# Kernel optimization log

Hardware: AMD Instinct MI355X
Metric: run time of the kernel (lower is better)

Reference implementation:

```python
import jax, jax.numpy as jnp
import numpy as np

N, G, NPG, K = 65536, 64, 1024, 32
NB, BD, IN_CH, GNN_DIM, L = 64, 4, 256, 256, 2
NBP = (BD - 1) * BD // 2 * NB  # 384
E = 524288


def setup_inputs():
    key = jax.random.key(0)
    ks = jax.random.split(key, 10)
    s = 0.05
    return {
        "x": jax.random.normal(ks[0], (N, IN_CH), jnp.float32),
        "eigvec": jax.random.normal(ks[1], (N, K), jnp.float32) / np.float32(np.sqrt(NPG)),
        "eigval": jax.random.uniform(ks[2], (G, K), jnp.float32, 0.0, 2.0),
        "taus": jnp.ones((NB,), jnp.float32),
        "enc_w": jax.random.normal(ks[3], (IN_CH, GNN_DIM), jnp.float32) * s,
        "enc_b": jnp.zeros((GNN_DIM,), jnp.float32),
        "self_w": jax.random.normal(ks[4], (L, GNN_DIM, GNN_DIM), jnp.float32) * s,
        "self_b": jnp.zeros((L, GNN_DIM), jnp.float32),
        "nb_w": jax.random.normal(ks[5], (L, GNN_DIM, GNN_DIM), jnp.float32) * s,
        "nb_b": jnp.zeros((L, GNN_DIM), jnp.float32),
        "dec_w": jax.random.normal(ks[6], (GNN_DIM, NBP), jnp.float32) * s,
        "dec_b": jnp.zeros((NBP,), jnp.float32),
        "lin_w": jax.random.normal(ks[7], (IN_CH, IN_CH), jnp.float32) * s,
        "lin_b": jnp.zeros((IN_CH,), jnp.float32),
        "edge_index": jax.random.randint(ks[8], (2, E), 0, N, jnp.int32),
    }


def _householder(p):
    # p: [M, BD*(BD-1)//2] -> Q: [M, BD, BD], product of BD-1 Householder reflectors
    M = p.shape[0]
    Q = jnp.broadcast_to(jnp.eye(BD, dtype=p.dtype), (M, BD, BD))
    idx = 0
    for j in range(BD - 1):  # small fixed loop over bundle_dim-1 reflectors
        n = BD - 1 - j
        v = jnp.zeros((M, BD), p.dtype).at[:, j].set(1.0)
        v = v.at[:, j + 1:].set(p[:, idx:idx + n])
        idx += n
        nrm = jnp.sum(v * v, axis=1)[:, None, None]
        Qv = jnp.einsum('mij,mj->mi', Q, v)
        Q = Q - 2.0 * Qv[:, :, None] * v[:, None, :] / nrm
    return Q


def reference(x, eigvec, eigval, taus, enc_w, enc_b, self_w, self_b,
              nb_w, nb_b, dec_w, dec_b, lin_w, lin_b, edge_index):
    gelu = lambda t: jax.nn.gelu(t, approximate=False)
    src, dst = edge_index[0], edge_index[1]
    vf = x.reshape(N, NB, BD, -1)                      # [N, NB, BD, 1]
    # SumGNN structural encoder: h = gelu(enc(x)); residual GNN layers; dec
    h = gelu(x @ enc_w + enc_b)
    for k in range(L):
        agg = jax.ops.segment_sum(h[src], dst, num_segments=N)  # sum aggregation
        hk = (h @ self_w[k] + self_b[k]) + (agg @ nb_w[k] + nb_b[k])
        h = gelu(hk) + h
    node_rep = h @ dec_w + dec_b                       # [N, NBP]
    Q = _householder(node_rep.reshape(N * NB, NBP // NB)).reshape(N, NB, BD, BD)
    vf = jnp.einsum('abcd,abde->abce', Q, vf)          # bundle transform
    h = vf.reshape(G, NPG, IN_CH)                      # to_dense_batch (equal-size graphs)
    ev = eigvec.reshape(G, NPG, K)
    hs = jnp.einsum('gnv,gnd->gvd', ev, h)             # project onto eigenbasis
    fact = jnp.exp(-eigval[:, :, None] * taus[None, None, :])   # [G, K, NB]
    hs = (hs.reshape(G, K, NB, BD, -1) * fact[..., None, None]).reshape(G, K, IN_CH)
    h = jnp.einsum('gnv,gvd->gnd', ev, hs).reshape(N, IN_CH)     # reproject
    h = h @ lin_w + lin_b
    vf = jnp.einsum('abdc,abde->abce', Q, h.reshape(N, NB, BD, -1))  # Q^T
    return vf.reshape(N, IN_CH)
```

## Files before the change

### kernel.cpp

```cpp
#include <hip/hip_runtime.h>
#include <math.h>

#define NN      65536
#define GG      64
#define NPG     1024
#define KEIG    32
#define NBUN    64
#define BDIM    4
#define CH      256
#define NBP     384
#define NEDGE   524288

using f16x8 = __attribute__((ext_vector_type(8))) _Float16;
using f16x4 = __attribute__((ext_vector_type(4))) _Float16;
using f32x4 = __attribute__((ext_vector_type(4))) float;

__device__ __forceinline__ float gelu_f(float x) {
    return 0.5f * x * (1.0f + erff(x * 0.70710678118654752440f));
}

template<int NOUT, int KTOT, bool DUAL, bool ACT, bool RESA, bool WF, bool W16>
__global__ __launch_bounds__(NOUT, 3) void mgemm_k(
    const _Float16* __restrict__ A1, const _Float16* __restrict__ A2,
    const _Float16* __restrict__ Bp, const float* __restrict__ bias,
    float* __restrict__ Cf, _Float16* __restrict__ C16)
{
    constexpr int NT   = KTOT / 32;
    constexpr int HALVES = KTOT / 256;
    constexpr int ROWB = 512;
    constexpr int CPR  = 32;
    constexpr int TOTC = 64 * CPR;
    constexpr int NSTG = TOTC / NOUT;
    constexpr int CTS  = NOUT + 8;
    constexpr int AH   = 64 * 256;
    constexpr int CTH  = 64 * CTS;
    constexpr int LDSH = (W16 && CTH > AH) ? CTH : AH;
    __shared__ _Float16 Alds[LDSH];

    const int tid  = threadIdx.x;
    const int lane = tid & 63;
    const int wave = tid >> 6;
    const int m0   = blockIdx.x * 64;

    const int r16 = lane & 15;
    const int kc  = lane >> 4;

    const _Float16* bpp = Bp + ((size_t)wave * NT * 2048) + lane * 8;

    f16x8 pa0, pa1, pa2, pa3, pb0, pb1, pb2, pb3;
    f16x8 pc0, pc1, pc2, pc3, pd0, pd1, pd2, pd3;

#define LDB(P0, P1, P2, P3, T)                                                 \
    {                                                                          \
        const _Float16* bq_ = bpp + (size_t)(T) * 2048;                        \
        P0 = *(const f16x8*)(bq_);                                             \
        P1 = *(const f16x8*)(bq_ + 512);                                       \
        P2 = *(const f16x8*)(bq_ + 1024);                                      \
        P3 = *(const f16x8*)(bq_ + 1536);                                      \
    }

    auto stage = [&](const _Float16* __restrict__ BASE) {
#pragma unroll
        for (int j0 = 0; j0 < NSTG; j0 += 4) {
            f16x8 s0, s1, s2, s3;
            const int nv = (NSTG - j0 >= 4) ? 4 : (NSTG - j0);
            int i0 = tid + (j0 + 0) * NOUT;
            int i1 = tid + (j0 + 1) * NOUT;
            int i2 = tid + (j0 + 2) * NOUT;
            int i3 = tid + (j0 + 3) * NOUT;
            if (nv > 0) s0 = *(const f16x8*)(BASE + (size_t)(m0 + (i0 >> 5)) * 256 + (i0 & 31) * 8);
            if (nv > 1) s1 = *(const f16x8*)(BASE + (size_t)(m0 + (i1 >> 5)) * 256 + (i1 & 31) * 8);
            if (nv > 2) s2 = *(const f16x8*)(BASE + (size_t)(m0 + (i2 >> 5)) * 256 + (i2 & 31) * 8);
            if (nv > 3) s3 = *(const f16x8*)(BASE + (size_t)(m0 + (i3 >> 5)) * 256 + (i3 & 31) * 8);
            if (nv > 0) *(f16x8*)((char*)Alds + ((((i0 >> 5) * ROWB + (i0 & 31) * 16)) ^ (((i0 >> 5) & 7) << 4))) = s0;
            if (nv > 1) *(f16x8*)((char*)Alds + ((((i1 >> 5) * ROWB + (i1 & 31) * 16)) ^ (((i1 >> 5) & 7) << 4))) = s1;
            if (nv > 2) *(f16x8*)((char*)Alds + ((((i2 >> 5) * ROWB + (i2 & 31) * 16)) ^ (((i2 >> 5) & 7) << 4))) = s2;
            if (nv > 3) *(f16x8*)((char*)Alds + ((((i3 >> 5) * ROWB + (i3 & 31) * 16)) ^ (((i3 >> 5) & 7) << 4))) = s3;
        }
        if (TOTC % NOUT) {
            const int idx = tid + NSTG * NOUT;
            if (idx < TOTC) {
                const int r = idx >> 5, c = idx & 31;
                f16x8 v = *(const f16x8*)(BASE + (size_t)(m0 + r) * 256 + c * 8);
                *(f16x8*)((char*)Alds + ((r * ROWB + c * 16) ^ ((r & 7) << 4))) = v;
            }
        }
    };

    LDB(pa0, pa1, pa2, pa3, 0)
    LDB(pb0, pb1, pb2, pb3, 1)
    LDB(pc0, pc1, pc2, pc3, 2)
    LDB(pd0, pd1, pd2, pd3, 3)

    stage(A1);
    __syncthreads();

    f32x4 acc[4][4];
#pragma unroll
    for (int i = 0; i < 4; i++)
#pragma unroll
        for (int j = 0; j < 4; j++) acc[i][j] = 0.f;

#define MSTEP(OFF, P0, P1, P2, P3)                                             \
    {                                                                          \
        const char* ap_ = (const char*)Alds + (OFF);                           \
        f16x8 a0_ = *(const f16x8*)(ap_);                                      \
        f16x8 a1_ = *(const f16x8*)(ap_ + 16 * ROWB);                          \
        f16x8 a2_ = *(const f16x8*)(ap_ + 32 * ROWB);                          \
        f16x8 a3_ = *(const f16x8*)(ap_ + 48 * ROWB);                          \
        acc[0][0] = __builtin_amdgcn_mfma_f32_16x16x32_f16(a0_, P0, acc[0][0], 0, 0, 0); \
        acc[0][1] = __builtin_amdgcn_mfma_f32_16x16x32_f16(a0_, P1, acc[0][1], 0, 0, 0); \
        acc[0][2] = __builtin_amdgcn_mfma_f32_16x16x32_f16(a0_, P2, acc[0][2], 0, 0, 0); \
        acc[0][3] = __builtin_amdgcn_mfma_f32_16x16x32_f16(a0_, P3, acc[0][3], 0, 0, 0); \
        acc[1][0] = __builtin_amdgcn_mfma_f32_16x16x32_f16(a1_, P0, acc[1][0], 0, 0, 0); \
        acc[1][1] = __builtin_amdgcn_mfma_f32_16x16x32_f16(a1_, P1, acc[1][1], 0, 0, 0); \
        acc[1][2] = __builtin_amdgcn_mfma_f32_16x16x32_f16(a1_, P2, acc[1][2], 0, 0, 0); \
        acc[1][3] = __builtin_amdgcn_mfma_f32_16x16x32_f16(a1_, P3, acc[1][3], 0, 0, 0); \
        acc[2][0] = __builtin_amdgcn_mfma_f32_16x16x32_f16(a2_, P0, acc[2][0], 0, 0, 0); \
        acc[2][1] = __builtin_amdgcn_mfma_f32_16x16x32_f16(a2_, P1, acc[2][1], 0, 0, 0); \
        acc[2][2] = __builtin_amdgcn_mfma_f32_16x16x32_f16(a2_, P2, acc[2][2], 0, 0, 0); \
        acc[2][3] = __builtin_amdgcn_mfma_f32_16x16x32_f16(a2_, P3, acc[2][3], 0, 0, 0); \
        acc[3][0] = __builtin_amdgcn_mfma_f32_16x16x32_f16(a3_, P0, acc[3][0], 0, 0, 0); \
        acc[3][1] = __builtin_amdgcn_mfma_f32_16x16x32_f16(a3_, P1, acc[3][1], 0, 0, 0); \
        acc[3][2] = __builtin_amdgcn_mfma_f32_16x16x32_f16(a3_, P2, acc[3][2], 0, 0, 0); \
        acc[3][3] = __builtin_amdgcn_mfma_f32_16x16x32_f16(a3_, P3, acc[3][3], 0, 0, 0); \
    }

    const int swz = (r16 & 7) << 4;
#pragma unroll
    for (int h = 0; h < HALVES; ++h) {
        if (h > 0) {
            __syncthreads();
            stage(A2);
            __syncthreads();
        }
        int au = r16 * ROWB + kc * 16;
#pragma unroll
        for (int tt = 0; tt < 8; tt += 4) {
            const int t = h * 8 + tt;
            MSTEP((au      ) ^ swz, pa0, pa1, pa2, pa3)
            if (t + 4 < NT) LDB(pa0, pa1, pa2, pa3, t + 4)
            MSTEP((au +  64) ^ swz, pb0, pb1, pb2, pb3)
            if (t + 5 < NT) LDB(pb0, pb1, pb2, pb3, t + 5)
            MSTEP((au + 128) ^ swz, pc0, pc1, pc2, pc3)
            if (t + 6 < NT) LDB(pc0, pc1, pc2, pc3, t + 6)
            MSTEP((au + 192) ^ swz, pd0, pd1, pd2, pd3)
            if (t + 7 < NT) LDB(pd0, pd1, pd2, pd3, t + 7)
            au += 256;
        }
    }
#undef LDB
#undef MSTEP

    const int rbase = (lane >> 4) * 4;
    const int ncol  = lane & 15;
    if constexpr (W16) {
        __syncthreads();
        constexpr int CPRN = NOUT / 8;
        constexpr int CPT  = 64 * CPRN / NOUT;
        f16x8 res[CPT];
        if constexpr (RESA) {
#pragma unroll
            for (int k2 = 0; k2 < CPT; k2++) {
                const int c = tid + k2 * NOUT;
                const int row = c / CPRN, col = c - row * CPRN;
                res[k2] = *(const f16x8*)(A1 + (size_t)(m0 + row) * 256 + col * 8);
            }
        }
#pragma unroll
        for (int nt = 0; nt < 4; nt++) {
            const int n = wave * 64 + nt * 16 + ncol;
            const float bs = bias[n];
#pragma unroll
            for (int mt = 0; mt < 4; mt++) {
#pragma unroll
                for (int i = 0; i < 4; i++) {
                    const int mr = mt * 16 + rbase + i;
                    float v = acc[mt][nt][i] + bs;
                    if (ACT) v = gelu_f(v);
                    Alds[mr * CTS + n] = (_Float16)v;
                }
            }
        }
        __syncthreads();
#pragma unroll
        for (int k2 = 0; k2 < CPT; k2++) {
            const int c = tid + k2 * NOUT;
            const int row = c / CPRN, col = c - row * CPRN;
            f16x8 v = *(const f16x8*)&Alds[row * CTS + col * 8];
            if constexpr (RESA) v = v + res[k2];
            *(f16x8*)(C16 + (size_t)(m0 + row) * NOUT + col * 8) = v;
        }
    } else {
#pragma unroll
        for (int nt = 0; nt < 4; nt++) {
            const int n = wave * 64 + nt * 16 + ncol;
            const float bs = bias[n];
#pragma unroll
            for (int mt = 0; mt < 4; mt++) {
#pragma unroll
                for (int i = 0; i < 4; i++) {
                    const int m = m0 + mt * 16 + rbase + i;
                    float v = acc[mt][nt][i] + bs;
                    if (ACT) v = gelu_f(v);
                    if (RESA) v += (float)A1[(size_t)m * 256 + n];
                    if (WF) Cf[(size_t)m * NOUT + n] = v;
                }
            }
        }
    }
}

template<int NOUT, int KTOT, bool DUAL>
__global__ __launch_bounds__(256) void pack_k(
    const float* __restrict__ W1, const float* __restrict__ W2,
    _Float16* __restrict__ Bp)
{
    constexpr int NT = KTOT / 32;
    const int cid = blockIdx.x * 256 + threadIdx.x;
    if (cid >= NOUT * KTOT / 8) return;
    const int l  = cid & 63;
    const int q  = (cid >> 6) & 3;
    const int c2 = cid >> 8;
    const int t  = c2 & (NT - 1);
    const int wn = c2 / NT;
    const int n  = wn * 64 + q * 16 + (l & 15);
    const int k0 = t * 32 + (l >> 4) * 8;
    f16x8 v;
#pragma unroll
    for (int j = 0; j < 8; j++) {
        const int k = k0 + j;
        float w = (DUAL && k >= 256) ? W2[(size_t)(k - 256) * NOUT + n]
                                     : W1[(size_t)k * NOUT + n];
        v[j] = (_Float16)w;
    }
    *(f16x8*)(Bp + (size_t)cid * 8) = v;
}

__global__ void zero_k(float* __restrict__ p, size_t n)
{
    size_t i = (size_t)blockIdx.x * blockDim.x + threadIdx.x;
    float4* p4 = (float4*)p;
    size_t n4 = n >> 2;
    for (size_t j = i; j < n4; j += (size_t)gridDim.x * blockDim.x)
        p4[j] = make_float4(0.f, 0.f, 0.f, 0.f);
}

__global__ __launch_bounds__(256) void cvt16_k(
    const float* __restrict__ in, _Float16* __restrict__ out)
{
    size_t i = (size_t)blockIdx.x * 256 + threadIdx.x;
    float4 v = ((const float4*)in)[i];
    f16x4 o = { (_Float16)v.x, (_Float16)v.y, (_Float16)v.z, (_Float16)v.w };
    ((f16x4*)out)[i] = o;
}

__global__ void bcomb_k(const float* __restrict__ a, const float* __restrict__ b,
                        float* __restrict__ o)
{
    int i = blockIdx.x * 256 + threadIdx.x;
    if (i < 512) o[i] = a[i] + b[i];
}

__global__ __launch_bounds__(256) void hist_k(const int* __restrict__ ei, int* __restrict__ deg)
{
    int e = blockIdx.x * 256 + threadIdx.x;
    if (e < NEDGE) atomicAdd(&deg[ei[NEDGE + e]], 1);
}

__global__ __launch_bounds__(1024) void scan_k(
    const int* __restrict__ deg, int* __restrict__ off, int* __restrict__ cursor)
{
    __shared__ int sh[1024];
    const int tid = threadIdx.x;
    const int base = tid * 64;
    int s = 0;
#pragma unroll 8
    for (int i = 0; i < 64; i++) s += deg[base + i];
    const int mysum = s;
    sh[tid] = s;
    __syncthreads();
    for (int ofs = 1; ofs < 1024; ofs <<= 1) {
        int v = (tid >= ofs) ? sh[tid - ofs] : 0;
        __syncthreads();
        sh[tid] += v;
        __syncthreads();
    }
    int running = sh[tid] - mysum;
    for (int i = 0; i < 64; i++) {
        off[base + i] = running;
        cursor[base + i] = running;
        running += deg[base + i];
    }
    if (tid == 1023) off[NN] = running;
}

__global__ __launch_bounds__(256) void fill_k(
    const int* __restrict__ ei, int* __restrict__ cursor, int* __restrict__ csr)
{
    int e = blockIdx.x * 256 + threadIdx.x;
    if (e < NEDGE) {
        int d = ei[NEDGE + e];
        int pos = atomicAdd(&cursor[d], 1);
        csr[pos] = ei[e];
    }
}

__global__ __launch_bounds__(256) void gather16_k(
    const _Float16* __restrict__ h, const int* __restrict__ off,
    const int* __restrict__ csr, _Float16* __restrict__ agg)
{
    const int lane = threadIdx.x & 63;
    const int n = blockIdx.x * 4 + (threadIdx.x >> 6);
    const int s0 = off[n], s1 = off[n + 1];
    float a0 = 0.f, a1 = 0.f, a2 = 0.f, a3 = 0.f;
    int j = s0;
    for (; j + 3 < s1; j += 4) {
        const int i0 = csr[j], i1 = csr[j + 1], i2 = csr[j + 2], i3 = csr[j + 3];
        f16x4 v0 = ((const f16x4*)(h + (size_t)i0 * CH))[lane];
        f16x4 v1 = ((const f16x4*)(h + (size_t)i1 * CH))[lane];
        f16x4 v2 = ((const f16x4*)(h + (size_t)i2 * CH))[lane];
        f16x4 v3 = ((const f16x4*)(h + (size_t)i3 * CH))[lane];
        a0 += (float)v0[0] + (float)v1[0] + (float)v2[0] + (float)v3[0];
        a1 += (float)v0[1] + (float)v1[1] + (float)v2[1] + (float)v3[1];
        a2 += (float)v0[2] + (float)v1[2] + (float)v2[2] + (float)v3[2];
        a3 += (float)v0[3] + (float)v1[3] + (float)v2[3] + (float)v3[3];
    }
    for (; j < s1; j++) {
        f16x4 va = ((const f16x4*)(h + (size_t)csr[j] * CH))[lane];
        a0 += (float)va[0]; a1 += (float)va[1]; a2 += (float)va[2]; a3 += (float)va[3];
    }
    f16x4 o = { (_Float16)a0, (_Float16)a1, (_Float16)a2, (_Float16)a3 };
    ((f16x4*)(agg + (size_t)n * CH))[lane] = o;
}

__device__ __forceinline__ void make_Q(const _Float16* __restrict__ p, float Q[4][4])
{
#pragma unroll
    for (int i = 0; i < 4; i++)
#pragma unroll
        for (int j = 0; j < 4; j++) Q[i][j] = (i == j) ? 1.f : 0.f;
    int idx = 0;
#pragma unroll
    for (int j = 0; j < 3; j++) {
        float v[4] = {0.f, 0.f, 0.f, 0.f};
        v[j] = 1.f;
#pragma unroll
        for (int t = 0; t < 4; t++)
            if (t > j) v[t] = (float)p[idx + t - (j + 1)];
        idx += 3 - j;
        float nrm = v[0]*v[0] + v[1]*v[1] + v[2]*v[2] + v[3]*v[3];
        float s = 2.f / nrm;
#pragma unroll
        for (int i = 0; i < 4; i++) {
            float qv = Q[i][0]*v[0] + Q[i][1]*v[1] + Q[i][2]*v[2] + Q[i][3]*v[3];
            float t0 = s * qv;
#pragma unroll
            for (int c = 0; c < 4; c++) Q[i][c] -= t0 * v[c];
        }
    }
}

template<bool TRANS>
__global__ __launch_bounds__(256) void bundle_k(
    const float* __restrict__ vin, const _Float16* __restrict__ nr,
    float* __restrict__ out)
{
    __shared__ _Float16 pb[4 * NBP];
    const int n0 = blockIdx.x * 4;
    for (int i = threadIdx.x; i < 4 * NBP; i += 256)
        pb[i] = nr[(size_t)n0 * NBP + i];
    __syncthreads();
    const int ln = threadIdx.x >> 6;
    const int b  = threadIdx.x & 63;
    const int n  = n0 + ln;
    float Q[4][4];
    make_Q(&pb[ln * NBP + b * 6], Q);
    float4 xv = ((const float4*)(vin + (size_t)n * CH))[b];
    float in0 = xv.x, in1 = xv.y, in2 = xv.z, in3 = xv.w;
    float4 o;
    if constexpr (!TRANS) {
        o.x = Q[0][0]*in0 + Q[0][1]*in1 + Q[0][2]*in2 + Q[0][3]*in3;
        o.y = Q[1][0]*in0 + Q[1][1]*in1 + Q[1][2]*in2 + Q[1][3]*in3;
        o.z = Q[2][0]*in0 + Q[2][1]*in1 + Q[2][2]*in2 + Q[2][3]*in3;
        o.w = Q[3][0]*in0 + Q[3][1]*in1 + Q[3][2]*in2 + Q[3][3]*in3;
    } else {
        o.x = Q[0][0]*in0 + Q[1][0]*in1 + Q[2][0]*in2 + Q[3][0]*in3;
        o.y = Q[0][1]*in0 + Q[1][1]*in1 + Q[2][1]*in2 + Q[3][1]*in3;
        o.z = Q[0][2]*in0 + Q[1][2]*in1 + Q[2][2]*in2 + Q[3][2]*in3;
        o.w = Q[0][3]*in0 + Q[1][3]*in1 + Q[2][3]*in2 + Q[3][3]*in3;
    }
    ((float4*)(out + (size_t)n * CH))[b] = o;
}

__global__ __launch_bounds__(256) void spec_proj_k(
    const float* __restrict__ v, const float* __restrict__ eigvec, float* __restrict__ hs)
{
    const int g = blockIdx.x;
    const int nbase = g * NPG + blockIdx.y * 128;
    __shared__ float evs[16][32];
    float acc[32];
#pragma unroll
    for (int k = 0; k < 32; k++) acc[k] = 0.f;
    for (int nt = 0; nt < 128; nt += 16) {
        __syncthreads();
        for (int i = threadIdx.x; i < 512; i += 256) {
            int nn = i >> 5, kk = i & 31;
            evs[nn][kk] = eigvec[(size_t)(nbase + nt + nn) * KEIG + kk];
        }
        __syncthreads();
#pragma unroll 4
        for (int nn = 0; nn < 16; nn++) {
            float hv = v[(size_t)(nbase + nt + nn) * CH + threadIdx.x];
#pragma unroll
            for (int k = 0; k < 32; k++) acc[k] += evs[nn][k] * hv;
        }
    }
    float* o = hs + (size_t)g * KEIG * CH + threadIdx.x;
#pragma unroll
    for (int k = 0; k < 32; k++) atomicAdd(o + k * CH, acc[k]);
}

__global__ __launch_bounds__(256) void spec_reproj16_k(
    const float* __restrict__ eigvec, const float* __restrict__ hs,
    const float* __restrict__ eigval, const float* __restrict__ taus,
    _Float16* __restrict__ out16)
{
    const int g = blockIdx.x >> 4;
    const int nbase = g * NPG + (blockIdx.x & 15) * 64;
    const float tau = taus[threadIdx.x >> 2];
    float hsr[32];
    const float* hg = hs + (size_t)g * KEIG * CH + threadIdx.x;
#pragma unroll
    for (int k = 0; k < 32; k++)
        hsr[k] = hg[k * CH] * expf(-eigval[g * KEIG + k] * tau);
    __shared__ float evs[64][32];
    for (int i = threadIdx.x; i < 2048; i += 256) {
        int nn = i >> 5, kk = i & 31;
        evs[nn][kk] = eigvec[(size_t)(nbase + nn) * KEIG + kk];
    }
    __syncthreads();
    for (int nn = 0; nn < 64; nn++) {
        float a = 0.f;
#pragma unroll
        for (int k = 0; k < 32; k++) a += evs[nn][k] * hsr[k];
        out16[(size_t)(nbase + nn) * CH + threadIdx.x] = (_Float16)a;
    }
}

extern "C" void kernel_launch(void* const* d_in, const int* in_sizes, int n_in,
                              void* d_out, int out_size, void* d_ws, size_t ws_size,
                              hipStream_t stream)
{
    const float* x      = (const float*)d_in[0];
    const float* eigvec = (const float*)d_in[1];
    const float* eigval = (const float*)d_in[2];
    const float* taus   = (const float*)d_in[3];
    const float* enc_w  = (const float*)d_in[4];
    const float* enc_b  = (const float*)d_in[5];
    const float* self_w = (const float*)d_in[6];
    const float* self_b = (const float*)d_in[7];
    const float* nb_w   = (const float*)d_in[8];
    const float* nb_b   = (const float*)d_in[9];
    const float* dec_w  = (const float*)d_in[10];
    const float* dec_b  = (const float*)d_in[11];
    const float* lin_w  = (const float*)d_in[12];
    const float* lin_b  = (const float*)d_in[13];
    const int*   ei     = (const int*)d_in[14];
    (void)in_sizes; (void)n_in; (void)out_size; (void)ws_size;

    float* ws = (float*)d_ws;
    _Float16* x16 = (_Float16*)(ws);
    _Float16* h0  = (_Float16*)(ws + 8388608);
    _Float16* h1  = (_Float16*)(ws + 16777216);
    _Float16* agg = (_Float16*)(ws + 25165824);
    int* ibase  = (int*)(ws + 33554432);
    int* deg    = ibase;
    int* off    = ibase + 65536;
    int* cursor = ibase + 131073;
    int* csr    = ibase + 196609;
    _Float16* nr16 = (_Float16*)(ws + 25165824);
    float* wb = ws + 37748752;
    _Float16* enc16 = (_Float16*)(wb);
    _Float16* l1w   = (_Float16*)(wb + 32768);
    _Float16* l2w   = (_Float16*)(wb + 98304);
    _Float16* dec16 = (_Float16*)(wb + 163840);
    _Float16* lin16 = (_Float16*)(wb + 212992);
    float* lbias = wb + 245760;
    _Float16* h2 = (_Float16*)(ws + 37995024);
    float* vf1 = ws;
    float* hs  = ws + 16777216;
    float* h3  = vf1;

    dim3 blk(256);

    cvt16_k<<<16384, blk, 0, stream>>>(x, x16);
    pack_k<256, 256, false><<<32, blk, 0, stream>>>(enc_w, nullptr, enc16);
    pack_k<256, 512, true ><<<64, blk, 0, stream>>>(self_w,         nb_w,         l1w);
    pack_k<256, 512, true ><<<64, blk, 0, stream>>>(self_w + 65536, nb_w + 65536, l2w);
    pack_k<384, 256, false><<<48, blk, 0, stream>>>(dec_w, nullptr, dec16);
    pack_k<256, 256, false><<<32, blk, 0, stream>>>(lin_w, nullptr, lin16);
    bcomb_k<<<2, blk, 0, stream>>>(self_b, nb_b, lbias);
    zero_k<<<64, blk, 0, stream>>>((float*)deg, (size_t)NN);
    hist_k<<<NEDGE / 256, blk, 0, stream>>>(ei, deg);
    scan_k<<<1, 1024, 0, stream>>>(deg, off, cursor);
    fill_k<<<NEDGE / 256, blk, 0, stream>>>(ei, cursor, csr);

    mgemm_k<256, 256, false, true, false, false, true><<<dim3(1024), blk, 0, stream>>>(
        x16, nullptr, enc16, enc_b, nullptr, h0);

    gather16_k<<<NN / 4, blk, 0, stream>>>(h0, off, csr, agg);
    mgemm_k<256, 512, true, true, true, false, true><<<dim3(1024), blk, 0, stream>>>(
        h0, agg, l1w, lbias, nullptr, h1);

    gather16_k<<<NN / 4, blk, 0, stream>>>(h1, off, csr, agg);
    mgemm_k<256, 512, true, true, true, false, true><<<dim3(1024), blk, 0, stream>>>(
        h1, agg, l2w, lbias + 256, nullptr, h0);

    mgemm_k<384, 256, false, false, false, false, true><<<dim3(1024), dim3(384), 0, stream>>>(
        h0, nullptr, dec16, dec_b, nullptr, nr16);

    bundle_k<false><<<NN / 4, blk, 0, stream>>>(x, nr16, vf1);

    zero_k<<<512, blk, 0, stream>>>(hs, (size_t)GG * KEIG * CH);
    spec_proj_k<<<dim3(GG, 8), blk, 0, stream>>>(vf1, eigvec, hs);
    spec_reproj16_k<<<GG * 16, blk, 0, stream>>>(eigvec, hs, eigval, taus, h2);

    mgemm_k<256, 256, false, false, false, true, false><<<dim3(1024), blk, 0, stream>>>(
        h2, nullptr, lin16, lin_b, h3, nullptr);

    bundle_k<true><<<NN / 4, blk, 0, stream>>>(h3, nr16, (float*)d_out);
}
```

Measured before the change: 688.5 us.

## Fuse fp32→fp16 conversion and bundle transforms into GEMM kernels

Removes the standalone x-to-fp16 conversion by loading fp32 A directly in the encoder GEMM. It fuses the forward bundle transform into the decoder GEMM epilogue, building Q from the tile still in LDS and writing vf as fp16. It also fuses the Q^T bundle transform into the final linear GEMM epilogue, staging fp32 results in LDS. This cuts several full-size global round trips and kernel launches. In exchange, the epilogues get heavier, LDS use grows, and the spectral projection now reads fp16 vf, which lowers precision.

Result: faster. 637.5 us (-7.4%).

```diff
diff --git a/kernel.cpp b/kernel.cpp
--- a/kernel.cpp
+++ b/kernel.cpp
@@ -19,11 +19,40 @@
     return 0.5f * x * (1.0f + erff(x * 0.70710678118654752440f));
 }
 
-template<int NOUT, int KTOT, bool DUAL, bool ACT, bool RESA, bool WF, bool W16>
+__device__ __forceinline__ void make_Q(const _Float16* __restrict__ p, float Q[4][4])
+{
+#pragma unroll
+    for (int i = 0; i < 4; i++)
+#pragma unroll
+        for (int j = 0; j < 4; j++) Q[i][j] = (i == j) ? 1.f : 0.f;
+    int idx = 0;
+#pragma unroll
+    for (int j = 0; j < 3; j++) {
+        float v[4] = {0.f, 0.f, 0.f, 0.f};
+        v[j] = 1.f;
+#pragma unroll
+        for (int t = 0; t < 4; t++)
+            if (t > j) v[t] = (float)p[idx + t - (j + 1)];
+        idx += 3 - j;
+        float nrm = v[0]*v[0] + v[1]*v[1] + v[2]*v[2] + v[3]*v[3];
+        float s = 2.f / nrm;
+#pragma unroll
+        for (int i = 0; i < 4; i++) {
+            float qv = Q[i][0]*v[0] + Q[i][1]*v[1] + Q[i][2]*v[2] + Q[i][3]*v[3];
+            float t0 = s * qv;
+#pragma unroll
+            for (int c = 0; c < 4; c++) Q[i][c] -= t0 * v[c];
+        }
+    }
+}
+
+template<int NOUT, int KTOT, bool DUAL, bool ACT, bool RESA, bool W16, bool A32, int BUN>
 __global__ __launch_bounds__(NOUT, 3) void mgemm_k(
     const _Float16* __restrict__ A1, const _Float16* __restrict__ A2,
-    const _Float16* __restrict__ Bp, const float* __restrict__ bias,
-    float* __restrict__ Cf, _Float16* __restrict__ C16)
+    const float* __restrict__ A1f, const _Float16* __restrict__ Bp,
+    const float* __restrict__ bias, _Float16* __restrict__ C16,
+    const float* __restrict__ xin, _Float16* __restrict__ vf16,
+    const _Float16* __restrict__ nrq, float* __restrict__ outf)
 {
     constexpr int NT   = KTOT / 32;
     constexpr int HALVES = KTOT / 256;
@@ -33,8 +62,10 @@
     constexpr int NSTG = TOTC / NOUT;
     constexpr int CTS  = NOUT + 8;
     constexpr int AH   = 64 * 256;
-    constexpr int CTH  = 64 * CTS;
-    constexpr int LDSH = (W16 && CTH > AH) ? CTH : AH;
+    constexpr int W16H = W16 ? 64 * CTS : 0;
+    constexpr int B2H  = (BUN == 2) ? 64 * CTS * 2 : 0;
+    constexpr int LDSH = (AH > W16H) ? ((AH > B2H) ? AH : B2H)
+                                     : ((W16H > B2H) ? W16H : B2H);
     __shared__ _Float16 Alds[LDSH];
 
     const int tid  = threadIdx.x;
@@ -59,7 +90,20 @@
         P3 = *(const f16x8*)(bq_ + 1536);                                      \
     }
 
-    auto stage = [&](const _Float16* __restrict__ BASE) {
+    auto ldA = [&](const _Float16* B16, const float* B32, int idx) -> f16x8 {
+        const size_t off = (size_t)(m0 + (idx >> 5)) * 256 + (idx & 31) * 8;
+        if constexpr (A32) {
+            float4 lo = *(const float4*)(B32 + off);
+            float4 hi = *(const float4*)(B32 + off + 4);
+            f16x8 r = { (_Float16)lo.x, (_Float16)lo.y, (_Float16)lo.z, (_Float16)lo.w,
+                        (_Float16)hi.x, (_Float16)hi.y, (_Float16)hi.z, (_Float16)hi.w };
+            return r;
+        } else {
+            return *(const f16x8*)(B16 + off);
+        }
+    };
+
+    auto stage = [&](const _Float16* B16, const float* B32) {
 #pragma unroll
         for (int j0 = 0; j0 < NSTG; j0 += 4) {
             f16x8 s0, s1, s2, s3;
@@ -68,10 +112,10 @@
             int i1 = tid + (j0 + 1) * NOUT;
             int i2 = tid + (j0 + 2) * NOUT;
             int i3 = tid + (j0 + 3) * NOUT;
-            if (nv > 0) s0 = *(const f16x8*)(BASE + (size_t)(m0 + (i0 >> 5)) * 256 + (i0 & 31) * 8);
-            if (nv > 1) s1 = *(const f16x8*)(BASE + (size_t)(m0 + (i1 >> 5)) * 256 + (i1 & 31) * 8);
-            if (nv > 2) s2 = *(const f16x8*)(BASE + (size_t)(m0 + (i2 >> 5)) * 256 + (i2 & 31) * 8);
-            if (nv > 3) s3 = *(const f16x8*)(BASE + (size_t)(m0 + (i3 >> 5)) * 256 + (i3 & 31) * 8);
+            if (nv > 0) s0 = ldA(B16, B32, i0);
+            if (nv > 1) s1 = ldA(B16, B32, i1);
+            if (nv > 2) s2 = ldA(B16, B32, i2);
+            if (nv > 3) s3 = ldA(B16, B32, i3);
             if (nv > 0) *(f16x8*)((char*)Alds + ((((i0 >> 5) * ROWB + (i0 & 31) * 16)) ^ (((i0 >> 5) & 7) << 4))) = s0;
             if (nv > 1) *(f16x8*)((char*)Alds + ((((i1 >> 5) * ROWB + (i1 & 31) * 16)) ^ (((i1 >> 5) & 7) << 4))) = s1;
             if (nv > 2) *(f16x8*)((char*)Alds + ((((i2 >> 5) * ROWB + (i2 & 31) * 16)) ^ (((i2 >> 5) & 7) << 4))) = s2;
@@ -80,8 +124,8 @@
         if (TOTC % NOUT) {
             const int idx = tid + NSTG * NOUT;
             if (idx < TOTC) {
+                f16x8 v = ldA(B16, B32, idx);
                 const int r = idx >> 5, c = idx & 31;
-                f16x8 v = *(const f16x8*)(BASE + (size_t)(m0 + r) * 256 + c * 8);
                 *(f16x8*)((char*)Alds + ((r * ROWB + c * 16) ^ ((r & 7) << 4))) = v;
             }
         }
@@ -92,7 +136,7 @@
     LDB(pc0, pc1, pc2, pc3, 2)
     LDB(pd0, pd1, pd2, pd3, 3)
 
-    stage(A1);
+    stage(A1, A1f);
     __syncthreads();
 
     f32x4 acc[4][4];
@@ -131,7 +175,7 @@
     for (int h = 0; h < HALVES; ++h) {
         if (h > 0) {
             __syncthreads();
-            stage(A2);
+            stage(A2, nullptr);
             __syncthreads();
         }
         int au = r16 * ROWB + kc * 16;
@@ -154,7 +198,36 @@
 
     const int rbase = (lane >> 4) * 4;
     const int ncol  = lane & 15;
-    if constexpr (W16) {
+    if constexpr (BUN == 2) {
+        __syncthreads();
+        float* Cl = (float*)Alds;
+        constexpr int CS4 = NOUT + 8;
+#pragma unroll
+        for (int nt = 0; nt < 4; nt++) {
+            const int n = wave * 64 + nt * 16 + ncol;
+            const float bs = bias[n];
+#pragma unroll
+            for (int mt = 0; mt < 4; mt++)
+#pragma unroll
+                for (int i = 0; i < 4; i++)
+                    Cl[(mt * 16 + rbase + i) * CS4 + n] = acc[mt][nt][i] + bs;
+        }
+        __syncthreads();
+#pragma unroll
+        for (int it = 0; it < 4096 / NOUT; it++) {
+            const int item = tid + it * NOUT;
+            const int row = item >> 6, b = item & 63;
+            float4 v = *(const float4*)&Cl[row * CS4 + b * 4];
+            float Q[4][4];
+            make_Q(nrq + (size_t)(m0 + row) * 384 + b * 6, Q);
+            float4 o;
+            o.x = Q[0][0]*v.x + Q[1][0]*v.y + Q[2][0]*v.z + Q[3][0]*v.w;
+            o.y = Q[0][1]*v.x + Q[1][1]*v.y + Q[2][1]*v.z + Q[3][1]*v.w;
+            o.z = Q[0][2]*v.x + Q[1][2]*v.y + Q[2][2]*v.z + Q[3][2]*v.w;
+            o.w = Q[0][3]*v.x + Q[1][3]*v.y + Q[2][3]*v.z + Q[3][3]*v.w;
+            *(float4*)(outf + (size_t)(m0 + row) * 256 + b * 4) = o;
+        }
+    } else {
         __syncthreads();
         constexpr int CPRN = NOUT / 8;
         constexpr int CPT  = 64 * CPRN / NOUT;
@@ -191,20 +264,22 @@
             if constexpr (RESA) v = v + res[k2];
             *(f16x8*)(C16 + (size_t)(m0 + row) * NOUT + col * 8) = v;
         }
-    } else {
-#pragma unroll
-        for (int nt = 0; nt < 4; nt++) {
-            const int n = wave * 64 + nt * 16 + ncol;
-            const float bs = bias[n];
-#pragma unroll
-            for (int mt = 0; mt < 4; mt++) {
-#pragma unroll
-                for (int i = 0; i < 4; i++) {
-                    const int m = m0 + mt * 16 + rbase + i;
-                    float v = acc[mt][nt][i] + bs;
-                    if (ACT) v = gelu_f(v);
-                    if (RESA) v += (float)A1[(size_t)m * 256 + n];
-                    if (WF) Cf[(size_t)m * NOUT + n] = v;
+        if constexpr (BUN == 1) {
+            constexpr int NIT = (4096 + NOUT - 1) / NOUT;
+#pragma unroll
+            for (int it = 0; it < NIT; it++) {
+                const int item = tid + it * NOUT;
+                if (item < 4096) {
+                    const int row = item >> 6, b = item & 63;
+                    float4 xv = *(const float4*)(xin + (size_t)(m0 + row) * 256 + b * 4);
+                    float Q[4][4];
+                    make_Q(&Alds[row * CTS + b * 6], Q);
+                    f16x4 o = {
+                        (_Float16)(Q[0][0]*xv.x + Q[0][1]*xv.y + Q[0][2]*xv.z + Q[0][3]*xv.w),
+                        (_Float16)(Q[1][0]*xv.x + Q[1][1]*xv.y + Q[1][2]*xv.z + Q[1][3]*xv.w),
+                        (_Float16)(Q[2][0]*xv.x + Q[2][1]*xv.y + Q[2][2]*xv.z + Q[2][3]*xv.w),
+                        (_Float16)(Q[3][0]*xv.x + Q[3][1]*xv.y + Q[3][2]*xv.z + Q[3][3]*xv.w) };
+                    *(f16x4*)(vf16 + (size_t)(m0 + row) * 256 + b * 4) = o;
                 }
             }
         }
@@ -244,15 +319,6 @@
     size_t n4 = n >> 2;
     for (size_t j = i; j < n4; j += (size_t)gridDim.x * blockDim.x)
         p4[j] = make_float4(0.f, 0.f, 0.f, 0.f);
-}
-
-__global__ __launch_bounds__(256) void cvt16_k(
-    const float* __restrict__ in, _Float16* __restrict__ out)
-{
-    size_t i = (size_t)blockIdx.x * 256 + threadIdx.x;
-    float4 v = ((const float4*)in)[i];
-    f16x4 o = { (_Float16)v.x, (_Float16)v.y, (_Float16)v.z, (_Float16)v.w };
-    ((f16x4*)out)[i] = o;
 }
 
 __global__ void bcomb_k(const float* __restrict__ a, const float* __restrict__ b,
@@ -334,67 +400,8 @@
     ((f16x4*)(agg + (size_t)n * CH))[lane] = o;
 }
 
-__device__ __forceinline__ void make_Q(const _Float16* __restrict__ p, float Q[4][4])
-{
-#pragma unroll
-    for (int i = 0; i < 4; i++)
-#pragma unroll
-        for (int j = 0; j < 4; j++) Q[i][j] = (i == j) ? 1.f : 0.f;
-    int idx = 0;
-#pragma unroll
-    for (int j = 0; j < 3; j++) {
-        float v[4] = {0.f, 0.f, 0.f, 0.f};
-        v[j] = 1.f;
-#pragma unroll
-        for (int t = 0; t < 4; t++)
-            if (t > j) v[t] = (float)p[idx + t - (j + 1)];
-        idx += 3 - j;
-        float nrm = v[0]*v[0] + v[1]*v[1] + v[2]*v[2] + v[3]*v[3];
-        float s = 2.f / nrm;
-#pragma unroll
-        for (int i = 0; i < 4; i++) {
-            float qv = Q[i][0]*v[0] + Q[i][1]*v[1] + Q[i][2]*v[2] + Q[i][3]*v[3];
-            float t0 = s * qv;
-#pragma unroll
-            for (int c = 0; c < 4; c++) Q[i][c] -= t0 * v[c];
-        }
-    }
-}
-
-template<bool TRANS>
-__global__ __launch_bounds__(256) void bundle_k(
-    const float* __restrict__ vin, const _Float16* __restrict__ nr,
-    float* __restrict__ out)
-{
-    __shared__ _Float16 pb[4 * NBP];
-    const int n0 = blockIdx.x * 4;
-    for (int i = threadIdx.x; i < 4 * NBP; i += 256)
-        pb[i] = nr[(size_t)n0 * NBP + i];
-    __syncthreads();
-    const int ln = threadIdx.x >> 6;
-    const int b  = threadIdx.x & 63;
-    const int n  = n0 + ln;
-    float Q[4][4];
-    make_Q(&pb[ln * NBP + b * 6], Q);
-    float4 xv = ((const float4*)(vin + (size_t)n * CH))[b];
-    float in0 = xv.x, in1 = xv.y, in2 = xv.z, in3 = xv.w;
-    float4 o;
-    if constexpr (!TRANS) {
-        o.x = Q[0][0]*in0 + Q[0][1]*in1 + Q[0][2]*in2 + Q[0][3]*in3;
-        o.y = Q[1][0]*in0 + Q[1][1]*in1 + Q[1][2]*in2 + Q[1][3]*in3;
-        o.z = Q[2][0]*in0 + Q[2][1]*in1 + Q[2][2]*in2 + Q[2][3]*in3;
-        o.w = Q[3][0]*in0 + Q[3][1]*in1 + Q[3][2]*in2 + Q[3][3]*in3;
-    } else {
-        o.x = Q[0][0]*in0 + Q[1][0]*in1 + Q[2][0]*in2 + Q[3][0]*in3;
-        o.y = Q[0][1]*in0 + Q[1][1]*in1 + Q[2][1]*in2 + Q[3][1]*in3;
-        o.z = Q[0][2]*in0 + Q[1][2]*in1 + Q[2][2]*in2 + Q[3][2]*in3;
-        o.w = Q[0][3]*in0 + Q[1][3]*in1 + Q[2][3]*in2 + Q[3][3]*in3;
-    }
-    ((float4*)(out + (size_t)n * CH))[b] = o;
-}
-
 __global__ __launch_bounds__(256) void spec_proj_k(
-    const float* __restrict__ v, const float* __restrict__ eigvec, float* __restrict__ hs)
+    const _Float16* __restrict__ v, const float* __restrict__ eigvec, float* __restrict__ hs)
 {
     const int g = blockIdx.x;
     const int nbase = g * NPG + blockIdx.y * 128;
@@ -411,7 +418,7 @@
         __syncthreads();
 #pragma unroll 4
         for (int nn = 0; nn < 16; nn++) {
-            float hv = v[(size_t)(nbase + nt + nn) * CH + threadIdx.x];
+            float hv = (float)v[(size_t)(nbase + nt + nn) * CH + threadIdx.x];
 #pragma unroll
             for (int k = 0; k < 32; k++) acc[k] += evs[nn][k] * hv;
         }
@@ -470,7 +477,6 @@
     (void)in_sizes; (void)n_in; (void)out_size; (void)ws_size;
 
     float* ws = (float*)d_ws;
-    _Float16* x16 = (_Float16*)(ws);
     _Float16* h0  = (_Float16*)(ws + 8388608);
     _Float16* h1  = (_Float16*)(ws + 16777216);
     _Float16* agg = (_Float16*)(ws + 25165824);
@@ -488,13 +494,11 @@
     _Float16* lin16 = (_Float16*)(wb + 212992);
     float* lbias = wb + 245760;
     _Float16* h2 = (_Float16*)(ws + 37995024);
-    float* vf1 = ws;
-    float* hs  = ws + 16777216;
-    float* h3  = vf1;
+    _Float16* vf16 = (_Float16*)(ws + 16777216);
+    float* hs  = ws;
 
     dim3 blk(256);
 
-    cvt16_k<<<16384, blk, 0, stream>>>(x, x16);
     pack_k<256, 256, false><<<32, blk, 0, stream>>>(enc_w, nullptr, enc16);
     pack_k<256, 512, true ><<<64, blk, 0, stream>>>(self_w,         nb_w,         l1w);
     pack_k<256, 512, true ><<<64, blk, 0, stream>>>(self_w + 65536, nb_w + 65536, l2w);
@@ -506,28 +510,24 @@
     scan_k<<<1, 1024, 0, stream>>>(deg, off, cursor);
     fill_k<<<NEDGE / 256, blk, 0, stream>>>(ei, cursor, csr);
 
-    mgemm_k<256, 256, false, true, false, false, true><<<dim3(1024), blk, 0, stream>>>(
-        x16, nullptr, enc16, enc_b, nullptr, h0);
+    mgemm_k<256, 256, false, true, false, true, true, 0><<<1024, blk, 0, stream>>>(
+        nullptr, nullptr, x, enc16, enc_b, h0, nullptr, nullptr, nullptr, nullptr);
 
     gather16_k<<<NN / 4, blk, 0, stream>>>(h0, off, csr, agg);
-    mgemm_k<256, 512, true, true, true, false, true><<<dim3(1024), blk, 0, stream>>>(
-        h0, agg, l1w, lbias, nullptr, h1);
+    mgemm_k<256, 512, true, true, true, true, false, 0><<<1024, blk, 0, stream>>>(
+        h0, agg, nullptr, l1w, lbias, h1, nullptr, nullptr, nullptr, nullptr);
 
     gather16_k<<<NN / 4, blk, 0, stream>>>(h1, off, csr, agg);
-    mgemm_k<256, 512, true, true, true, false, true><<<dim3(1024), blk, 0, stream>>>(
-        h1, agg, l2w, lbias + 256, nullptr, h0);
-
-    mgemm_k<384, 256, false, false, false, false, true><<<dim3(1024), dim3(384), 0, stream>>>(
-        h0, nullptr, dec16, dec_b, nullptr, nr16);
-
-    bundle_k<false><<<NN / 4, blk, 0, stream>>>(x, nr16, vf1);
+    mgemm_k<256, 512, true, true, true, true, false, 0><<<1024, blk, 0, stream>>>(
+        h1, agg, nullptr, l2w, lbias + 256, h0, nullptr, nullptr, nullptr, nullptr);
+
+    mgemm_k<384, 256, false, false, false, true, false, 1><<<1024, dim3(384), 0, stream>>>(
+        h0, nullptr, nullptr, dec16, dec_b, nr16, x, vf16, nullptr, nullptr);
 
     zero_k<<<512, blk, 0, stream>>>(hs, (size_t)GG * KEIG * CH);
-    spec_proj_k<<<dim3(GG, 8), blk, 0, stream>>>(vf1, eigvec, hs);
+    spec_proj_k<<<dim3(GG, 8), blk, 0, stream>>>(vf16, eigvec, hs);
     spec_reproj16_k<<<GG * 16, blk, 0, stream>>>(eigvec, hs, eigval, taus, h2);
 
-    mgemm_k<256, 256, false, false, false, true, false><<<dim3(1024), blk, 0, stream>>>(
-        h2, nullptr, lin16, lin_b, h3, nullptr);
-
-    bundle_k<true><<<NN / 4, blk, 0, stream>>>(h3, nr16, (float*)d_out);
-}
+    mgemm_k<256, 256, false, false, false, false, false, 2><<<1024, blk, 0, stream>>>(
+        h2, nullptr, nullptr, lin16, lin_b, nullptr, nullptr, nullptr, nr16, (float*)d_out);
+}
```
